# Kernel tuning notes

Hardware: AMD Instinct MI355X
Metric: run time of the kernel (lower is better)

The kernel has to match this reference:

```python
import jax, jax.numpy as jnp
import numpy as np

N, D = 1024, 512
BS, N_TEXT, N_VIDEO = 64, 16, 16
BETA = 1.0
N_ITERS = 50


def setup_inputs() -> dict:
    key = jax.random.key(0)
    k1, k2 = jax.random.split(key)
    return {
        "t_prob": jax.random.normal(k1, (N, D), dtype=jnp.float32),
        "v_prob": jax.random.normal(k2, (N, D), dtype=jnp.float32),
        "n": N,
        "bs": BS,
        "n_text": N_TEXT,
        "n_video": N_VIDEO,
    }


def _l2norm(x):
    # matches F.normalize(x, p=2, dim=1) (eps irrelevant for randn inputs)
    return x / jnp.linalg.norm(x, axis=1, keepdims=True)


def reference(t_prob, v_prob, n, bs, n_text, n_video):
    dt = t_prob.dtype
    x = _l2norm(t_prob)
    y = _l2norm(v_prob)
    C = 1.0 - x @ y.T                      # [n, n] cosine distance
    A = jnp.exp(-C / BETA)

    sigma0 = jnp.ones((n, 1), dtype=dt) / n
    T0 = jnp.ones((n, n), dtype=dt)

    def step(carry, _):
        T, sigma = carry
        Q = A * T                          # [n, n]
        delta = 1.0 / (n * (Q @ sigma))    # [n, 1]
        sigma_new = 1.0 / (n * (Q.T @ delta))  # [n, 1]
        # diag(delta) @ Q @ diag(sigma) == row/col rescale
        T_new = delta * Q * sigma_new.T
        return (T_new, sigma_new), None

    (T, _), _ = jax.lax.scan(step, (T0, sigma0), None, length=N_ITERS)

    distance_matrix = C.T @ T              # [n, n]
    distance_matrix = distance_matrix.reshape(bs, n_text, bs, n_video).mean(axis=(1, 3))
    dis_loss = jnp.trace(distance_matrix)
    return distance_matrix, dis_loss
```

## Files before the change

### kernel.cpp

```cpp
#include <hip/hip_runtime.h>
#include <math.h>


#define NWG 32
#define TPB 1024
#define NIT 50
#define NREP 4

typedef unsigned long long ull;

constexpr int CL_OFF   = 0;
constexpr int CVEC_OFF = 1024 * 1024;
constexpr int CNT_OFF  = CVEC_OFF + 3 * NREP * 1024;

__global__ __launch_bounds__(512) void k_gemm(const float* __restrict__ X,
                                              const float* __restrict__ Y,
                                              float* __restrict__ ws) {
    __shared__ float As[32][68];
    __shared__ float Bs[32][68];
    __shared__ float nX[64], nY[64];
    float* Cl = ws + CL_OFF;

    int tid = threadIdx.x;
    int tx = tid & 31, ty = tid >> 5;
    int bx = blockIdx.x, by = blockIdx.y;
    int lr0 = tid >> 3;
    int kq  = (tid & 7) * 4;

    float acc[4][2] = {};
    float sx = 0.f, sy = 0.f;
    for (int k0 = 0; k0 < 512; k0 += 32) {
        float4 xa = *(const float4*)(X + (size_t)(by * 64 + lr0) * 512 + k0 + kq);
        float4 ya = *(const float4*)(Y + (size_t)(bx * 64 + lr0) * 512 + k0 + kq);
        sx += xa.x * xa.x + xa.y * xa.y + xa.z * xa.z + xa.w * xa.w;
        sy += ya.x * ya.x + ya.y * ya.y + ya.z * ya.z + ya.w * ya.w;
        As[kq + 0][lr0] = xa.x; As[kq + 1][lr0] = xa.y;
        As[kq + 2][lr0] = xa.z; As[kq + 3][lr0] = xa.w;
        Bs[kq + 0][lr0] = ya.x; Bs[kq + 1][lr0] = ya.y;
        Bs[kq + 2][lr0] = ya.z; Bs[kq + 3][lr0] = ya.w;
        __syncthreads();
#pragma unroll
        for (int kk = 0; kk < 32; ++kk) {
            float4 a4 = *(const float4*)&As[kk][4 * ty];
            float2 b2 = *(const float2*)&Bs[kk][2 * tx];
            float av[4] = {a4.x, a4.y, a4.z, a4.w};
#pragma unroll
            for (int r = 0; r < 4; ++r) {
                acc[r][0] += av[r] * b2.x;
                acc[r][1] += av[r] * b2.y;
            }
        }
        __syncthreads();
    }
#pragma unroll
    for (int m = 1; m < 8; m <<= 1) {
        sx += __shfl_xor(sx, m, 64);
        sy += __shfl_xor(sy, m, 64);
    }
    if ((tid & 7) == 0) { nX[lr0] = sx; nY[lr0] = sy; }
    __syncthreads();

    int i0 = by * 64 + 4 * ty, j0 = bx * 64 + 2 * tx;
    float vy0 = 1.0f / sqrtf(nY[2 * tx + 0]);
    float vy1 = 1.0f / sqrtf(nY[2 * tx + 1]);
#pragma unroll
    for (int r = 0; r < 4; ++r) {
        float vx = 1.0f / sqrtf(nX[4 * ty + r]);
        float2 o;
        o.x = acc[r][0] * vx * vy0 - 1.0f;
        o.y = acc[r][1] * vx * vy1 - 1.0f;
        *(float2*)(Cl + (size_t)(i0 + r) * 1024 + j0) = o;
    }
}

__global__ __launch_bounds__(1024)
__attribute__((amdgpu_waves_per_eu(1, 4)))
void k_ipot(float* __restrict__ ws, float* __restrict__ out) {
    __shared__ float sLp[1056];
    __shared__ float buf[16 * 1056];
    __shared__ float twv[16];
    __shared__ float pad[2600];

    const int g = blockIdx.x, tid = threadIdx.x;
    const int rs = tid >> 6, lane = tid & 63;
    const int uo = tid & 15, lo = tid >> 4;
    float* Cl   = ws + CL_OFF;
    float* cvec = ws + CVEC_OFF;
    unsigned* grp = (unsigned*)(ws + CNT_OFF);

    pad[tid & 2047] = 0.0f;

    const float* csrc0 = Cl + (size_t)(g * 32 + rs * 2 + 0) * 1024 + lane * 16;
    const float* csrc1 = csrc0 + 1024;

    float E[2][16];
    float p0 = 0.0f, p1 = 0.0f;
#pragma unroll
    for (int q = 0; q < 4; ++q) {
        float4 c0 = *(const float4*)(csrc0 + 4 * q);
        float4 c1 = *(const float4*)(csrc1 + 4 * q);
        p0 += c0.x + c0.y + c0.z + c0.w;
        p1 += c1.x + c1.y + c1.z + c1.w;
        E[0][4 * q + 0] = __expf(c0.x); E[0][4 * q + 1] = __expf(c0.y);
        E[0][4 * q + 2] = __expf(c0.z); E[0][4 * q + 3] = __expf(c0.w);
        E[1][4 * q + 0] = __expf(c1.x); E[1][4 * q + 1] = __expf(c1.y);
        E[1][4 * q + 2] = __expf(c1.z); E[1][4 * q + 3] = __expf(c1.w);
    }

    float bv = 1.0f;
    float a0 = 0.0f, a1 = 0.0f;

    for (int t = 0; t < NIT; ++t) {
        float sval;
        if (t == 0) {
            sval = 1.0f / 1024.0f;
        } else {
            if (tid == 0) {
                unsigned tgt = (unsigned)t * 8u;
                long gd = 0;
                while (__hip_atomic_load(&grp[0], __ATOMIC_RELAXED, __HIP_MEMORY_SCOPE_AGENT) < tgt ||
                       __hip_atomic_load(&grp[1], __ATOMIC_RELAXED, __HIP_MEMORY_SCOPE_AGENT) < tgt ||
                       __hip_atomic_load(&grp[2], __ATOMIC_RELAXED, __HIP_MEMORY_SCOPE_AGENT) < tgt ||
                       __hip_atomic_load(&grp[3], __ATOMIC_RELAXED, __HIP_MEMORY_SCOPE_AGENT) < tgt) {
                    __builtin_amdgcn_s_sleep(1);
                    if (++gd > 2000000) break;
                }
            }
            __syncthreads();
            const float* rb = cvec + ((t + 2) % 3) * (NREP * 1024) + tid;
            float r0 = __hip_atomic_load(rb + 0 * 1024, __ATOMIC_RELAXED, __HIP_MEMORY_SCOPE_AGENT);
            float r1 = __hip_atomic_load(rb + 1 * 1024, __ATOMIC_RELAXED, __HIP_MEMORY_SCOPE_AGENT);
            float r2 = __hip_atomic_load(rb + 2 * 1024, __ATOMIC_RELAXED, __HIP_MEMORY_SCOPE_AGENT);
            float r3 = __hip_atomic_load(rb + 3 * 1024, __ATOMIC_RELAXED, __HIP_MEMORY_SCOPE_AGENT);
            if (t >= 2 && tid < 64) {
                ull* zb = (ull*)(cvec + ((t + 1) % 3) * (NREP * 1024)) + g * 64 + tid;
                __hip_atomic_store(zb, 0ull, __ATOMIC_RELAXED, __HIP_MEMORY_SCOPE_AGENT);
            }
            float c = r0 + r1 + r2 + r3;
            float b = 1.0f / c;
            sval = b * b / bv * (1.0f / 1024.0f);
            bv = b;
        }
        sLp[uo * 66 + lo] = sval;
        __syncthreads();

        float sv[16];
#pragma unroll
        for (int u = 0; u < 16; ++u) sv[u] = sLp[u * 66 + lane];
        float rp0 = 0.0f, rp1 = 0.0f;
#pragma unroll
        for (int u = 0; u < 16; ++u) {
            rp0 += E[0][u] * sv[u];
            rp1 += E[1][u] * sv[u];
        }
#pragma unroll
        for (int m = 1; m < 64; m <<= 1) {
            rp0 += __shfl_xor(rp0, m, 64);
            rp1 += __shfl_xor(rp1, m, 64);
        }
        a0 = 1.0f / (1024.0f * rp0);
        a1 = 1.0f / (1024.0f * rp1);

#pragma unroll
        for (int u = 0; u < 16; ++u)
            buf[rs * 1056 + u * 66 + lane] = E[0][u] * a0 + E[1][u] * a1;
        __syncthreads();

        float csum = 0.0f;
#pragma unroll
        for (int w = 0; w < 16; ++w) csum += buf[w * 1056 + uo * 66 + lo];
        atomicAdd(cvec + (t % 3) * (NREP * 1024) + (g & 3) * 1024 + tid, csum);
        __syncthreads();
        if (tid == 0)
            __hip_atomic_fetch_add(&grp[g >> 3], 1u, __ATOMIC_RELAXED,
                                   __HIP_MEMORY_SCOPE_AGENT);

        if (t < NIT - 1) {
            const float kf = (float)(t + 2);
#pragma unroll
            for (int q = 0; q < 4; ++q) {
                float4 c0 = *(const float4*)(csrc0 + 4 * q);
                float4 c1 = *(const float4*)(csrc1 + 4 * q);
                E[0][4 * q + 0] = __expf(kf * c0.x); E[0][4 * q + 1] = __expf(kf * c0.y);
                E[0][4 * q + 2] = __expf(kf * c0.z); E[0][4 * q + 3] = __expf(kf * c0.w);
                E[1][4 * q + 0] = __expf(kf * c1.x); E[1][4 * q + 1] = __expf(kf * c1.y);
                E[1][4 * q + 2] = __expf(kf * c1.z); E[1][4 * q + 3] = __expf(kf * c1.w);
            }
        }
    }

    if (tid == 0) {
        unsigned tgt = (unsigned)NIT * 8u;
        long gd = 0;
        while (__hip_atomic_load(&grp[0], __ATOMIC_RELAXED, __HIP_MEMORY_SCOPE_AGENT) < tgt ||
               __hip_atomic_load(&grp[1], __ATOMIC_RELAXED, __HIP_MEMORY_SCOPE_AGENT) < tgt ||
               __hip_atomic_load(&grp[2], __ATOMIC_RELAXED, __HIP_MEMORY_SCOPE_AGENT) < tgt ||
               __hip_atomic_load(&grp[3], __ATOMIC_RELAXED, __HIP_MEMORY_SCOPE_AGENT) < tgt) {
            __builtin_amdgcn_s_sleep(1);
            if (++gd > 2000000) break;
        }
    }
    __syncthreads();
    {
        const float* rb = cvec + ((NIT - 1) % 3) * (NREP * 1024) + tid;
        float r0 = __hip_atomic_load(rb + 0 * 1024, __ATOMIC_RELAXED, __HIP_MEMORY_SCOPE_AGENT);
        float r1 = __hip_atomic_load(rb + 1 * 1024, __ATOMIC_RELAXED, __HIP_MEMORY_SCOPE_AGENT);
        float r2 = __hip_atomic_load(rb + 2 * 1024, __ATOMIC_RELAXED, __HIP_MEMORY_SCOPE_AGENT);
        float r3 = __hip_atomic_load(rb + 3 * 1024, __ATOMIC_RELAXED, __HIP_MEMORY_SCOPE_AGENT);
        sLp[uo * 66 + lo] = 1.0f / (r0 + r1 + r2 + r3);
    }
    __syncthreads();

    float* Ps = buf;
    float* Rs = buf + 2048;
    float bl[16];
#pragma unroll
    for (int u = 0; u < 16; ++u) bl[u] = sLp[u * 66 + lane];
    {
        float r0 = 0.0f, r1 = 0.0f;
#pragma unroll
        for (int u = 0; u < 16; ++u) {
            r0 += E[0][u] * bl[u];
            r1 += E[1][u] * bl[u];
        }
        Ps[(rs * 2 + 0) * 64 + lane] = -p0;
        Rs[(rs * 2 + 0) * 64 + lane] = a0 * r0;
        Ps[(rs * 2 + 1) * 64 + lane] = -p1;
        Rs[(rs * 2 + 1) * 64 + lane] = a1 * r1;
    }
    __syncthreads();

    float Rk[32];
#pragma unroll
    for (int k = 0; k < 32; ++k) Rk[k] = Rs[k * 64 + lane];
    const float sc = 1.0f / (256.0f * 1024.0f);
    float tsum = pad[tid & 2047];
#pragma unroll
    for (int q = 0; q < 4; ++q) {
        int o = tid + 1024 * q;
        int A = o >> 6;
        float acc = 0.0f;
#pragma unroll
        for (int k = 0; k < 32; ++k) acc += Ps[k * 64 + A] * Rk[k];
        float val = acc * sc;
        atomicAdd(out + o, val);
        if (A == lane) tsum += val;
    }
#pragma unroll
    for (int m = 1; m < 64; m <<= 1) tsum += __shfl_xor(tsum, m, 64);
    if (lane == 0) twv[rs] = tsum;
    __syncthreads();
    if (tid == 0) {
        float ts = 0.0f;
#pragma unroll
        for (int w = 0; w < 16; ++w) ts += twv[w];
        atomicAdd(out + 4096, ts);
    }
}

extern "C" void kernel_launch(void* const* d_in, const int* in_sizes, int n_in,
                              void* d_out, int out_size, void* d_ws, size_t ws_size,
                              hipStream_t stream) {
    const float* X = (const float*)d_in[0];
    const float* Y = (const float*)d_in[1];
    float* out = (float*)d_out;
    float* ws  = (float*)d_ws;

    (void)hipMemsetAsync((char*)d_ws + (size_t)CVEC_OFF * 4, 0,
                         (size_t)(3 * NREP * 1024 + 16) * 4, stream);
    (void)hipMemsetAsync(d_out, 0, (size_t)out_size * 4, stream);

    k_gemm<<<dim3(16, 16), 512, 0, stream>>>(X, Y, ws);
    k_ipot<<<NWG, TPB, 0, stream>>>(ws, out);
}
```

Baseline: 332.0 us.

## Use per-block flags for grid barrier, widen atomic replicas, retile gemm to 1024 threads

The grid barrier changes from four shared group counters, polled serially by one thread, to one flag per workgroup. A whole wavefront polls all 32 flags in parallel and tests them with __all. The atomic-accumulation replica count for column sums goes from 4 to 8 to cut contention on each address. The GEMM kernel moves to 1024 threads with a 2x2 per-thread tile, and the waves_per_eu attribute is dropped from the iterative kernel. These aim to lower the per-iteration barrier latency and the atomic serialization. In exchange, each iteration does more loads and zeroing of replicas.

Result: slower. 352.8 us (+6.3%).

```diff
diff --git a/kernel.cpp b/kernel.cpp
--- a/kernel.cpp
+++ b/kernel.cpp
@@ -5,67 +5,62 @@
 #define NWG 32
 #define TPB 1024
 #define NIT 50
-#define NREP 4
+#define NREP 8
 
 typedef unsigned long long ull;
 
 constexpr int CL_OFF   = 0;
 constexpr int CVEC_OFF = 1024 * 1024;
-constexpr int CNT_OFF  = CVEC_OFF + 3 * NREP * 1024;
-
-__global__ __launch_bounds__(512) void k_gemm(const float* __restrict__ X,
-                                              const float* __restrict__ Y,
-                                              float* __restrict__ ws) {
+constexpr int FLG_OFF  = CVEC_OFF + 3 * NREP * 1024;
+
+__global__ __launch_bounds__(1024) void k_gemm(const float* __restrict__ X,
+                                               const float* __restrict__ Y,
+                                               float* __restrict__ ws) {
     __shared__ float As[32][68];
     __shared__ float Bs[32][68];
     __shared__ float nX[64], nY[64];
     float* Cl = ws + CL_OFF;
 
     int tid = threadIdx.x;
+    int bx = blockIdx.x, by = blockIdx.y;
+
+    int st  = tid & 511;
+    int lr0 = st >> 3;
+    int kq  = (st & 7) * 4;
+    const bool isX = tid < 512;
+    const float* SRC = isX ? X : Y;
+    int rcb = (isX ? by : bx) * 64;
+
     int tx = tid & 31, ty = tid >> 5;
-    int bx = blockIdx.x, by = blockIdx.y;
-    int lr0 = tid >> 3;
-    int kq  = (tid & 7) * 4;
-
-    float acc[4][2] = {};
-    float sx = 0.f, sy = 0.f;
+    float acc[2][2] = {};
+    float sn = 0.f;
     for (int k0 = 0; k0 < 512; k0 += 32) {
-        float4 xa = *(const float4*)(X + (size_t)(by * 64 + lr0) * 512 + k0 + kq);
-        float4 ya = *(const float4*)(Y + (size_t)(bx * 64 + lr0) * 512 + k0 + kq);
-        sx += xa.x * xa.x + xa.y * xa.y + xa.z * xa.z + xa.w * xa.w;
-        sy += ya.x * ya.x + ya.y * ya.y + ya.z * ya.z + ya.w * ya.w;
-        As[kq + 0][lr0] = xa.x; As[kq + 1][lr0] = xa.y;
-        As[kq + 2][lr0] = xa.z; As[kq + 3][lr0] = xa.w;
-        Bs[kq + 0][lr0] = ya.x; Bs[kq + 1][lr0] = ya.y;
-        Bs[kq + 2][lr0] = ya.z; Bs[kq + 3][lr0] = ya.w;
+        float4 v = *(const float4*)(SRC + (size_t)(rcb + lr0) * 512 + k0 + kq);
+        sn += v.x * v.x + v.y * v.y + v.z * v.z + v.w * v.w;
+        float (*S)[68] = isX ? As : Bs;
+        S[kq + 0][lr0] = v.x; S[kq + 1][lr0] = v.y;
+        S[kq + 2][lr0] = v.z; S[kq + 3][lr0] = v.w;
         __syncthreads();
 #pragma unroll
         for (int kk = 0; kk < 32; ++kk) {
-            float4 a4 = *(const float4*)&As[kk][4 * ty];
+            float2 a2 = *(const float2*)&As[kk][2 * ty];
             float2 b2 = *(const float2*)&Bs[kk][2 * tx];
-            float av[4] = {a4.x, a4.y, a4.z, a4.w};
-#pragma unroll
-            for (int r = 0; r < 4; ++r) {
-                acc[r][0] += av[r] * b2.x;
-                acc[r][1] += av[r] * b2.y;
-            }
-        }
-        __syncthreads();
-    }
-#pragma unroll
-    for (int m = 1; m < 8; m <<= 1) {
-        sx += __shfl_xor(sx, m, 64);
-        sy += __shfl_xor(sy, m, 64);
-    }
-    if ((tid & 7) == 0) { nX[lr0] = sx; nY[lr0] = sy; }
-    __syncthreads();
-
-    int i0 = by * 64 + 4 * ty, j0 = bx * 64 + 2 * tx;
+            acc[0][0] += a2.x * b2.x; acc[0][1] += a2.x * b2.y;
+            acc[1][0] += a2.y * b2.x; acc[1][1] += a2.y * b2.y;
+        }
+        __syncthreads();
+    }
+#pragma unroll
+    for (int m = 1; m < 8; m <<= 1) sn += __shfl_xor(sn, m, 64);
+    if ((st & 7) == 0) { if (isX) nX[lr0] = sn; else nY[lr0] = sn; }
+    __syncthreads();
+
+    int i0 = by * 64 + 2 * ty, j0 = bx * 64 + 2 * tx;
     float vy0 = 1.0f / sqrtf(nY[2 * tx + 0]);
     float vy1 = 1.0f / sqrtf(nY[2 * tx + 1]);
 #pragma unroll
-    for (int r = 0; r < 4; ++r) {
-        float vx = 1.0f / sqrtf(nX[4 * ty + r]);
+    for (int r = 0; r < 2; ++r) {
+        float vx = 1.0f / sqrtf(nX[2 * ty + r]);
         float2 o;
         o.x = acc[r][0] * vx * vy0 - 1.0f;
         o.y = acc[r][1] * vx * vy1 - 1.0f;
@@ -74,7 +69,6 @@
 }
 
 __global__ __launch_bounds__(1024)
-__attribute__((amdgpu_waves_per_eu(1, 4)))
 void k_ipot(float* __restrict__ ws, float* __restrict__ out) {
     __shared__ float sLp[1056];
     __shared__ float buf[16 * 1056];
@@ -86,7 +80,7 @@
     const int uo = tid & 15, lo = tid >> 4;
     float* Cl   = ws + CL_OFF;
     float* cvec = ws + CVEC_OFF;
-    unsigned* grp = (unsigned*)(ws + CNT_OFF);
+    unsigned* flg = (unsigned*)(ws + FLG_OFF);
 
     pad[tid & 2047] = 0.0f;
 
@@ -115,15 +109,16 @@
         if (t == 0) {
             sval = 1.0f / 1024.0f;
         } else {
-            if (tid == 0) {
-                unsigned tgt = (unsigned)t * 8u;
+            if (rs == 0) {
+                const unsigned* fb = flg + (lane & 31);
+                const unsigned tgt = (unsigned)t;
                 long gd = 0;
-                while (__hip_atomic_load(&grp[0], __ATOMIC_RELAXED, __HIP_MEMORY_SCOPE_AGENT) < tgt ||
-                       __hip_atomic_load(&grp[1], __ATOMIC_RELAXED, __HIP_MEMORY_SCOPE_AGENT) < tgt ||
-                       __hip_atomic_load(&grp[2], __ATOMIC_RELAXED, __HIP_MEMORY_SCOPE_AGENT) < tgt ||
-                       __hip_atomic_load(&grp[3], __ATOMIC_RELAXED, __HIP_MEMORY_SCOPE_AGENT) < tgt) {
+                for (;;) {
+                    unsigned v = __hip_atomic_load(fb, __ATOMIC_RELAXED,
+                                                   __HIP_MEMORY_SCOPE_AGENT);
+                    if (__all(v >= tgt)) break;
+                    if (++gd > 2000000) break;
                     __builtin_amdgcn_s_sleep(1);
-                    if (++gd > 2000000) break;
                 }
             }
             __syncthreads();
@@ -132,11 +127,15 @@
             float r1 = __hip_atomic_load(rb + 1 * 1024, __ATOMIC_RELAXED, __HIP_MEMORY_SCOPE_AGENT);
             float r2 = __hip_atomic_load(rb + 2 * 1024, __ATOMIC_RELAXED, __HIP_MEMORY_SCOPE_AGENT);
             float r3 = __hip_atomic_load(rb + 3 * 1024, __ATOMIC_RELAXED, __HIP_MEMORY_SCOPE_AGENT);
-            if (t >= 2 && tid < 64) {
-                ull* zb = (ull*)(cvec + ((t + 1) % 3) * (NREP * 1024)) + g * 64 + tid;
+            float r4 = __hip_atomic_load(rb + 4 * 1024, __ATOMIC_RELAXED, __HIP_MEMORY_SCOPE_AGENT);
+            float r5 = __hip_atomic_load(rb + 5 * 1024, __ATOMIC_RELAXED, __HIP_MEMORY_SCOPE_AGENT);
+            float r6 = __hip_atomic_load(rb + 6 * 1024, __ATOMIC_RELAXED, __HIP_MEMORY_SCOPE_AGENT);
+            float r7 = __hip_atomic_load(rb + 7 * 1024, __ATOMIC_RELAXED, __HIP_MEMORY_SCOPE_AGENT);
+            if (t >= 2 && tid < 128) {
+                ull* zb = (ull*)(cvec + ((t + 1) % 3) * (NREP * 1024)) + g * 128 + tid;
                 __hip_atomic_store(zb, 0ull, __ATOMIC_RELAXED, __HIP_MEMORY_SCOPE_AGENT);
             }
-            float c = r0 + r1 + r2 + r3;
+            float c = r0 + r1 + r2 + r3 + r4 + r5 + r6 + r7;
             float b = 1.0f / c;
             sval = b * b / bv * (1.0f / 1024.0f);
             bv = b;
@@ -169,11 +168,11 @@
         float csum = 0.0f;
 #pragma unroll
         for (int w = 0; w < 16; ++w) csum += buf[w * 1056 + uo * 66 + lo];
-        atomicAdd(cvec + (t % 3) * (NREP * 1024) + (g & 3) * 1024 + tid, csum);
+        atomicAdd(cvec + (t % 3) * (NREP * 1024) + (g & 7) * 1024 + tid, csum);
         __syncthreads();
         if (tid == 0)
-            __hip_atomic_fetch_add(&grp[g >> 3], 1u, __ATOMIC_RELAXED,
-                                   __HIP_MEMORY_SCOPE_AGENT);
+            __hip_atomic_store(&flg[g], (unsigned)(t + 1),
+                               __ATOMIC_RELAXED, __HIP_MEMORY_SCOPE_AGENT);
 
         if (t < NIT - 1) {
             const float kf = (float)(t + 2);
@@ -189,15 +188,15 @@
         }
     }
 
-    if (tid == 0) {
-        unsigned tgt = (unsigned)NIT * 8u;
+    if (rs == 0) {
+        const unsigned* fb = flg + (lane & 31);
         long gd = 0;
-        while (__hip_atomic_load(&grp[0], __ATOMIC_RELAXED, __HIP_MEMORY_SCOPE_AGENT) < tgt ||
-               __hip_atomic_load(&grp[1], __ATOMIC_RELAXED, __HIP_MEMORY_SCOPE_AGENT) < tgt ||
-               __hip_atomic_load(&grp[2], __ATOMIC_RELAXED, __HIP_MEMORY_SCOPE_AGENT) < tgt ||
-               __hip_atomic_load(&grp[3], __ATOMIC_RELAXED, __HIP_MEMORY_SCOPE_AGENT) < tgt) {
+        for (;;) {
+            unsigned v = __hip_atomic_load(fb, __ATOMIC_RELAXED,
+                                           __HIP_MEMORY_SCOPE_AGENT);
+            if (__all(v >= (unsigned)NIT)) break;
+            if (++gd > 2000000) break;
             __builtin_amdgcn_s_sleep(1);
-            if (++gd > 2000000) break;
         }
     }
     __syncthreads();
@@ -207,7 +206,11 @@
         float r1 = __hip_atomic_load(rb + 1 * 1024, __ATOMIC_RELAXED, __HIP_MEMORY_SCOPE_AGENT);
         float r2 = __hip_atomic_load(rb + 2 * 1024, __ATOMIC_RELAXED, __HIP_MEMORY_SCOPE_AGENT);
         float r3 = __hip_atomic_load(rb + 3 * 1024, __ATOMIC_RELAXED, __HIP_MEMORY_SCOPE_AGENT);
-        sLp[uo * 66 + lo] = 1.0f / (r0 + r1 + r2 + r3);
+        float r4 = __hip_atomic_load(rb + 4 * 1024, __ATOMIC_RELAXED, __HIP_MEMORY_SCOPE_AGENT);
+        float r5 = __hip_atomic_load(rb + 5 * 1024, __ATOMIC_RELAXED, __HIP_MEMORY_SCOPE_AGENT);
+        float r6 = __hip_atomic_load(rb + 6 * 1024, __ATOMIC_RELAXED, __HIP_MEMORY_SCOPE_AGENT);
+        float r7 = __hip_atomic_load(rb + 7 * 1024, __ATOMIC_RELAXED, __HIP_MEMORY_SCOPE_AGENT);
+        sLp[uo * 66 + lo] = 1.0f / (r0 + r1 + r2 + r3 + r4 + r5 + r6 + r7);
     }
     __syncthreads();
 
@@ -267,9 +270,9 @@
     float* ws  = (float*)d_ws;
 
     (void)hipMemsetAsync((char*)d_ws + (size_t)CVEC_OFF * 4, 0,
-                         (size_t)(3 * NREP * 1024 + 16) * 4, stream);
+                         (size_t)(3 * NREP * 1024 + 64) * 4, stream);
     (void)hipMemsetAsync(d_out, 0, (size_t)out_size * 4, stream);
 
-    k_gemm<<<dim3(16, 16), 512, 0, stream>>>(X, Y, ws);
+    k_gemm<<<dim3(16, 16), 1024, 0, stream>>>(X, Y, ws);
     k_ipot<<<NWG, TPB, 0, stream>>>(ws, out);
 }
```
